# Performance work log

Hardware: AMD Instinct MI355X
Metric: run time of the kernel (lower is better)

## Reference

```python
import jax, jax.numpy as jnp
import numpy as np

N = 30000   # nodes
E = 480000  # edges
IN = 128    # hidden_dim (in_feats)
H = 4       # num_heads
D = 128     # out_feats per head
HD = H * D
NEG_SLOPE = 0.2
BN_EPS = 1e-5


def setup_inputs() -> dict:
    key = jax.random.key(0)
    ks = jax.random.split(key, 12)
    feat = jax.random.normal(ks[0], (N, IN), dtype=jnp.float32)
    src = jax.random.randint(ks[1], (E,), 0, N)
    dst = jax.random.randint(ks[2], (E,), 0, N)
    sc_in = 1.0 / np.sqrt(IN)
    sc_hd = 1.0 / np.sqrt(HD)
    W_fc = jax.random.normal(ks[3], (IN, HD), dtype=jnp.float32) * sc_in
    attn_l = jax.random.normal(ks[4], (H, D), dtype=jnp.float32) * sc_in
    attn_r = jax.random.normal(ks[5], (H, D), dtype=jnp.float32) * sc_in
    W_res = jax.random.normal(ks[6], (IN, HD), dtype=jnp.float32) * sc_in
    bias_gat = jnp.zeros((HD,), dtype=jnp.float32)
    gamma = jnp.ones((HD,), dtype=jnp.float32)
    beta = jnp.zeros((HD,), dtype=jnp.float32)
    W_out = jax.random.normal(ks[7], (HD, IN), dtype=jnp.float32) * sc_hd
    b_out = jnp.zeros((IN,), dtype=jnp.float32)
    return dict(feat=feat, src=src, dst=dst, W_fc=W_fc, attn_l=attn_l,
                attn_r=attn_r, W_res=W_res, bias_gat=bias_gat,
                gamma=gamma, beta=beta, W_out=W_out, b_out=b_out)


def reference(feat, src, dst, W_fc, attn_l, attn_r, W_res, bias_gat,
              gamma, beta, W_out, b_out):
    # --- GATConv (eval mode: dropout off) ---
    h = (feat @ W_fc).reshape(N, H, D)               # projected feats [N,H,D]
    el = jnp.einsum('nhd,hd->nh', h, attn_l)         # [N,H]
    er = jnp.einsum('nhd,hd->nh', h, attn_r)         # [N,H]
    e = el[src] + er[dst]                            # [E,H]
    e = jnp.where(e > 0, e, NEG_SLOPE * e)           # leaky_relu(0.2)
    # segment softmax over edges grouped by destination node
    emax = jax.ops.segment_max(e, dst, num_segments=N)   # [N,H]
    emax = jnp.where(jnp.isfinite(emax), emax, 0.0)      # empty segments
    ex = jnp.exp(e - emax[dst])                          # [E,H]
    denom = jax.ops.segment_sum(ex, dst, num_segments=N) # [N,H]
    a = ex / denom[dst]                                  # [E,H] attention
    msgs = h[src] * a[:, :, None]                        # [E,H,D]
    rst = jax.ops.segment_sum(msgs, dst, num_segments=N) # [N,H,D]
    # residual (in_feats != H*out_feats -> linear res_fc) + bias
    rst = rst + (feat @ W_res).reshape(N, H, D) + bias_gat.reshape(1, H, D)
    # --- fc_out: Flatten -> BatchNorm1d (train stats) -> ReLU -> Linear ---
    x = rst.reshape(N, HD)
    mu = x.mean(axis=0)
    var = x.var(axis=0)
    xn = (x - mu) / jnp.sqrt(var + BN_EPS)
    x = jnp.maximum(gamma * xn + beta, 0.0)
    return x @ W_out + b_out                             # [N, IN]
```

## Files before the change

kernel.cpp:

```cpp
#include <hip/hip_runtime.h>

#define N_  30000
#define E_  480000

typedef short short8 __attribute__((ext_vector_type(8)));
typedef float f32x4  __attribute__((ext_vector_type(4)));
typedef unsigned int u32x4 __attribute__((ext_vector_type(4)));
typedef unsigned int u32x2 __attribute__((ext_vector_type(2)));
union Frag { u32x4 q; short8 v; unsigned short us[8]; };

__device__ __forceinline__ float b2f(unsigned short u){
  union { unsigned int i; float f; } v; v.i = ((unsigned int)u) << 16; return v.f;
}
__device__ __forceinline__ float blo(unsigned int u){
  union { unsigned int i; float f; } v; v.i = u << 16; return v.f;
}
__device__ __forceinline__ float bhi(unsigned int u){
  union { unsigned int i; float f; } v; v.i = u & 0xffff0000u; return v.f;
}
__device__ __forceinline__ unsigned short f2b(float f){
  union { float f; unsigned int u; } v; v.f = f;
  unsigned int u = v.u;
  return (unsigned short)((u + 0x7fffu + ((u >> 16) & 1u)) >> 16);
}

__global__ void k_initconv(const float* __restrict__ Wfc, const float* __restrict__ Wres,
                           const float* __restrict__ Wout, const float* __restrict__ feat,
                           unsigned short* __restrict__ Wt2, unsigned short* __restrict__ WtOut,
                           unsigned short* __restrict__ featb,
                           int* __restrict__ counts, int* __restrict__ cursor){
  int gid = blockIdx.x * 256 + threadIdx.x;
  int stride = gridDim.x * 256;
  if (gid < N_){ counts[gid] = 0; cursor[gid] = 0; }
  const int total1 = 512 * 256;
  const int total2 = 128 * 512;
  for (int i = gid; i < total1 + total2; i += stride){
    if (i < total1){
      int c = i >> 8, k = i & 255;
      float v = (k < 128) ? Wfc[k * 512 + c] : Wres[(k - 128) * 512 + c];
      Wt2[c * 256 + k] = f2b(v);
    } else {
      int j = i - total1;
      int n = j >> 9, k = j & 511;
      WtOut[n * 512 + k] = f2b(Wout[k * 128 + n]);
    }
  }
  for (int i = gid; i < N_ * 128; i += stride)
    featb[i] = f2b(feat[i]);
}

__global__ __launch_bounds__(128) void k_prep(const float* __restrict__ Wfc,
                                              const float* __restrict__ al,
                                              const float* __restrict__ ar,
                                              float* __restrict__ P){
  int idx = blockIdx.x * 128 + threadIdx.x;
  if (idx >= 1024) return;
  int k = idx >> 3, q = idx & 7;
  int h = q & 3;
  const float* a = (q < 4) ? al : ar;
  const float* wr = Wfc + k * 512 + h * 128;
  const float* av = a + h * 128;
  float s = 0.f;
#pragma unroll 4
  for (int d = 0; d < 128; d++) s += wr[d] * av[d];
  P[k * 8 + q] = s;
}

__global__ __launch_bounds__(256) void k_el(const float* __restrict__ feat,
                                            const float* __restrict__ P,
                                            float* __restrict__ el, float* __restrict__ er){
  __shared__ float sF[32 * 132];
  __shared__ float sP[1024];
  int t = threadIdx.x;
  int n0 = blockIdx.x * 32;
  *reinterpret_cast<f32x4*>(&sP[t * 4]) = *reinterpret_cast<const f32x4*>(P + t * 4);
#pragma unroll
  for (int i = 0; i < 4; i++){
    int c = t + i * 256;
    int r = c >> 5, cw = (c & 31) * 4;
    int gn = n0 + r;
    f32x4 v = {0.f, 0.f, 0.f, 0.f};
    if (gn < N_) v = *reinterpret_cast<const f32x4*>(feat + gn * 128 + cw);
    *reinterpret_cast<f32x4*>(&sF[r * 132 + cw]) = v;
  }
  __syncthreads();
  int node = t >> 3, q = t & 7;
  int gn = n0 + node;
  const float* fr = &sF[node * 132];
  float s = 0.f;
#pragma unroll 2
  for (int k = 0; k < 128; k += 4){
    f32x4 fv = *reinterpret_cast<const f32x4*>(fr + k);
#pragma unroll
    for (int j = 0; j < 4; j++) s += fv[j] * sP[(k + j) * 8 + q];
  }
  if (gn < N_){
    if (q < 4) el[gn * 4 + q] = s;
    else       er[gn * 4 + (q - 4)] = s;
  }
}

__global__ void k_hist(const int* __restrict__ dst, int* __restrict__ counts){
  int e = blockIdx.x * 256 + threadIdx.x;
  if (e < E_) atomicAdd(&counts[dst[e]], 1);
}

__global__ __launch_bounds__(1024) void k_scan(const int* __restrict__ counts,
                                               int* __restrict__ offs){
  __shared__ int wsum[16];
  int t = threadIdx.x;
  int lane = t & 63, w = t >> 6;
  int base = t * 32;
  int vals[32];
  int s = 0;
#pragma unroll
  for (int j = 0; j < 32; j++){
    int idx = base + j;
    int v = (idx < N_) ? counts[idx] : 0;
    vals[j] = s;
    s += v;
  }
  int x = s;
  for (int o = 1; o < 64; o <<= 1){
    int y = __shfl_up(x, o);
    if (lane >= o) x += y;
  }
  if (lane == 63) wsum[w] = x;
  __syncthreads();
  if (t < 16){
    int y = wsum[t];
    for (int o = 1; o < 16; o <<= 1){
      int z = __shfl_up(y, o, 16);
      if (t >= o) y += z;
    }
    wsum[t] = y;
  }
  __syncthreads();
  int wbase = (w > 0) ? wsum[w - 1] : 0;
  int ex = wbase + x - s;
#pragma unroll
  for (int j = 0; j < 32; j++){
    int idx = base + j;
    if (idx <= N_) offs[idx] = ex + vals[j];
  }
}

__global__ void k_edge(const int* __restrict__ src, const int* __restrict__ dst,
                       const float* __restrict__ el, const float* __restrict__ er,
                       float* __restrict__ es_s, int* __restrict__ src_s,
                       const int* __restrict__ offs, int* __restrict__ cursor){
  int e = blockIdx.x * 256 + threadIdx.x;
  if (e >= E_) return;
  int s = src[e], d = dst[e];
  f32x4 a = *reinterpret_cast<const f32x4*>(el + s * 4);
  f32x4 b = *reinterpret_cast<const f32x4*>(er + d * 4);
  f32x4 v = a + b;
#pragma unroll
  for (int i = 0; i < 4; i++) v[i] = v[i] > 0.f ? v[i] : 0.2f * v[i];
  int p = atomicAdd(&cursor[d], 1);
  int pos = offs[d] + p;
  *reinterpret_cast<f32x4*>(es_s + pos * 4) = v;
  src_s[pos] = s;
}

__global__ __launch_bounds__(256) void k_soft(const int* __restrict__ offs,
                                              float* __restrict__ es_s){
  int wave = threadIdx.x >> 6, lane = threadIdx.x & 63;
  int n = blockIdx.x * 4 + wave;
  if (n >= N_) return;
  int head = lane >> 4, sub = lane & 15;
  int off0 = offs[n], g = offs[n + 1] - off0;
  float m = -1e30f;
  for (int i = sub; i < g; i += 16)
    m = fmaxf(m, es_s[(off0 + i) * 4 + head]);
  for (int o = 8; o >= 1; o >>= 1) m = fmaxf(m, __shfl_xor(m, o, 16));
  float ss = 0.f;
  for (int i = sub; i < g; i += 16)
    ss += __expf(es_s[(off0 + i) * 4 + head] - m);
  for (int o = 8; o >= 1; o >>= 1) ss += __shfl_xor(ss, o, 16);
  float rd = (ss > 0.f) ? 1.0f / ss : 0.f;
  for (int i = sub; i < g; i += 16){
    int idx = (off0 + i) * 4 + head;
    es_s[idx] = __expf(es_s[idx] - m) * rd;
  }
}

__global__ __launch_bounds__(256) void k_aggrf(const int* __restrict__ offs,
                                               const int* __restrict__ src_s,
                                               const float* __restrict__ w,
                                               const unsigned short* __restrict__ featb,
                                               unsigned short* __restrict__ fagg){
  int wave = threadIdx.x >> 6, lane = threadIdx.x & 63;
  int n = blockIdx.x * 4 + wave;
  if (n >= N_) return;
  int off0 = __builtin_amdgcn_readfirstlane(offs[n]);
  int g = __builtin_amdgcn_readfirstlane(offs[n + 1]) - off0;
  int c0 = lane * 2;
  float acc[4][2] = {};
  int i = 0;
  for (; i + 7 < g; i += 8){
    int s8[8];
    f32x4 w8[8];
    unsigned int p8[8];
#pragma unroll
    for (int u = 0; u < 8; u++) s8[u] = __builtin_amdgcn_readfirstlane(src_s[off0 + i + u]);
#pragma unroll
    for (int u = 0; u < 8; u++) w8[u] = *reinterpret_cast<const f32x4*>(w + (off0 + i + u) * 4);
#pragma unroll
    for (int u = 0; u < 8; u++) p8[u] = *reinterpret_cast<const unsigned int*>(featb + s8[u] * 128 + c0);
#pragma unroll
    for (int u = 0; u < 8; u++){
      float lo = blo(p8[u]), hi = bhi(p8[u]);
#pragma unroll
      for (int h = 0; h < 4; h++){
        acc[h][0] += w8[u][h] * lo;
        acc[h][1] += w8[u][h] * hi;
      }
    }
  }
  for (; i < g; i++){
    int sv = __builtin_amdgcn_readfirstlane(src_s[off0 + i]);
    f32x4 wv = *reinterpret_cast<const f32x4*>(w + (off0 + i) * 4);
    unsigned int pv = *reinterpret_cast<const unsigned int*>(featb + sv * 128 + c0);
    float lo = blo(pv), hi = bhi(pv);
#pragma unroll
    for (int h = 0; h < 4; h++){
      acc[h][0] += wv[h] * lo;
      acc[h][1] += wv[h] * hi;
    }
  }
#pragma unroll
  for (int h = 0; h < 4; h++){
    unsigned int ov = (unsigned int)f2b(acc[h][0]) | ((unsigned int)f2b(acc[h][1]) << 16);
    *reinterpret_cast<unsigned int*>(fagg + n * 512 + h * 128 + c0) = ov;
  }
}

__global__ __launch_bounds__(256) void k_gemmC(const unsigned short* __restrict__ fagg,
                                               const unsigned short* __restrict__ featb,
                                               const unsigned short* __restrict__ Wt2,
                                               const float* __restrict__ bias,
                                               unsigned short* __restrict__ comb){
  __shared__ unsigned short wsl[256 * 40];
  int tid = threadIdx.x;
  int wave = tid >> 6, lane = tid & 63;
  int lrow = lane & 15, quad = lane >> 4;
  int rowbase = blockIdx.x * 64 + wave * 16;
  int colbase = blockIdx.y * 256;
  int h0 = blockIdx.y * 2;
  int arow = rowbase + lrow; if (arow > N_ - 1) arow = N_ - 1;
  const unsigned short* aF = fagg + arow * 512 + h0 * 128;
  const unsigned short* aX = featb + arow * 128;
  f32x4 acc[16] = {};
  for (int kk = 0; kk < 8; kk++){
    __syncthreads();
#pragma unroll
    for (int i = 0; i < 4; i++){
      int c = tid + i * 256;
      int col = c >> 2, w = (c & 3) * 8;
      u32x4 v = *reinterpret_cast<const u32x4*>(Wt2 + (colbase + col) * 256 + kk * 32 + w);
      *reinterpret_cast<u32x4*>(&wsl[col * 40 + w]) = v;
    }
    __syncthreads();
    Frag a0, a1;
    if (kk < 4){
      a0.q = *reinterpret_cast<const u32x4*>(aF + kk * 32 + quad * 8);
      a1.q = *reinterpret_cast<const u32x4*>(aF + 128 + kk * 32 + quad * 8);
    } else {
      a0.q = *reinterpret_cast<const u32x4*>(aX + (kk - 4) * 32 + quad * 8);
      a1.q = a0.q;
    }
#pragma unroll
    for (int s = 0; s < 16; s++){
      Frag b; b.q = *reinterpret_cast<const u32x4*>(&wsl[(s * 16 + lrow) * 40 + quad * 8]);
      acc[s] = __builtin_amdgcn_mfma_f32_16x16x32_bf16(b.v, (s < 8 ? a0.v : a1.v), acc[s], 0, 0, 0);
    }
  }
  int gr = rowbase + lrow;
  if (gr < N_){
    unsigned short* crow = comb + gr * 512 + colbase;
#pragma unroll
    for (int s = 0; s < 16; s++){
      int cb = colbase + s * 16 + quad * 4;
      f32x4 bb = *reinterpret_cast<const f32x4*>(bias + cb);
      u32x2 ov;
#pragma unroll
      for (int d = 0; d < 2; d++){
        float v0 = acc[s][2 * d]     + bb[2 * d];
        float v1 = acc[s][2 * d + 1] + bb[2 * d + 1];
        ov[d] = (unsigned int)f2b(v0) | ((unsigned int)f2b(v1) << 16);
      }
      *reinterpret_cast<u32x2*>(crow + s * 16 + quad * 4) = ov;
    }
  }
}

__global__ __launch_bounds__(256) void k_stats(const unsigned short* __restrict__ comb,
                                               float* __restrict__ psum,
                                               float* __restrict__ psq){
  __shared__ float lsum[4][512];
  __shared__ float lsq[4][512];
  int t = threadIdx.x, lane = t & 63, rg = t >> 6;
  int c0 = lane * 8;
  const int rows = 118;
  int r0 = blockIdx.x * rows;
  int r1 = r0 + rows; if (r1 > N_) r1 = N_;
  float s[8] = {}, q[8] = {};
  for (int r = r0 + rg; r < r1; r += 4){
    u32x4 pv = *reinterpret_cast<const u32x4*>(comb + r * 512 + c0);
#pragma unroll
    for (int d = 0; d < 4; d++){
      float v0 = blo(pv[d]);
      float v1 = bhi(pv[d]);
      s[2*d]   += v0; q[2*d]   += v0 * v0;
      s[2*d+1] += v1; q[2*d+1] += v1 * v1;
    }
  }
#pragma unroll
  for (int d = 0; d < 8; d++){ lsum[rg][c0 + d] = s[d]; lsq[rg][c0 + d] = q[d]; }
  __syncthreads();
#pragma unroll
  for (int half = 0; half < 2; half++){
    int ch = t + half * 256;
    float a = lsum[0][ch] + lsum[1][ch] + lsum[2][ch] + lsum[3][ch];
    float b = lsq[0][ch] + lsq[1][ch] + lsq[2][ch] + lsq[3][ch];
    psum[blockIdx.x * 512 + ch] = a;
    psq[blockIdx.x * 512 + ch] = b;
  }
}

__global__ __launch_bounds__(128) void k_bnfin(const float* __restrict__ psum,
                                               const float* __restrict__ psq,
                                               const float* __restrict__ gamma,
                                               const float* __restrict__ beta,
                                               float* __restrict__ scale,
                                               float* __restrict__ shift){
  int ch = blockIdx.x * 128 + threadIdx.x;
  float s0 = 0.f, s1 = 0.f, s2 = 0.f, s3 = 0.f;
  float q0 = 0.f, q1 = 0.f, q2 = 0.f, q3 = 0.f;
  for (int b = 0; b < 256; b += 4){
    s0 += psum[(b    ) * 512 + ch];
    s1 += psum[(b + 1) * 512 + ch];
    s2 += psum[(b + 2) * 512 + ch];
    s3 += psum[(b + 3) * 512 + ch];
    q0 += psq[(b    ) * 512 + ch];
    q1 += psq[(b + 1) * 512 + ch];
    q2 += psq[(b + 2) * 512 + ch];
    q3 += psq[(b + 3) * 512 + ch];
  }
  float sum = (s0 + s1) + (s2 + s3);
  float sq  = (q0 + q1) + (q2 + q3);
  float mu  = sum / (float)N_;
  float var = sq / (float)N_ - mu * mu;
  float inv = rsqrtf(var + 1e-5f);
  float sc  = gamma[ch] * inv;
  scale[ch] = sc;
  shift[ch] = beta[ch] - mu * sc;
}

__global__ __launch_bounds__(256) void k_gemm2(const unsigned short* __restrict__ comb,
                                               const unsigned short* __restrict__ WtOut,
                                               const float* __restrict__ scale,
                                               const float* __restrict__ shift,
                                               const float* __restrict__ bout,
                                               float* __restrict__ out){
  __shared__ float sc[512], sh[512];
  __shared__ unsigned short wsl[128 * 40];
  int t = threadIdx.x;
  for (int i = t; i < 512; i += 256){ sc[i] = scale[i]; sh[i] = shift[i]; }
  int wave = t >> 6, lane = t & 63, lrow = lane & 15, quad = lane >> 4;
  int rowbase = blockIdx.x * 64 + wave * 16;
  int rr = rowbase + lrow; if (rr > N_ - 1) rr = N_ - 1;
  const unsigned short* arow = comb + rr * 512;
  f32x4 acc[8] = {};
  for (int kk = 0; kk < 16; kk++){
    __syncthreads();
#pragma unroll
    for (int i = 0; i < 2; i++){
      int c = t + i * 256;
      int col = c >> 2, w = (c & 3) * 8;
      u32x4 v = *reinterpret_cast<const u32x4*>(WtOut + col * 512 + kk * 32 + w);
      *reinterpret_cast<u32x4*>(&wsl[col * 40 + w]) = v;
    }
    __syncthreads();
    int base = kk * 32 + quad * 8;
    Frag a; a.q = *reinterpret_cast<const u32x4*>(arow + base);
#pragma unroll
    for (int i2 = 0; i2 < 8; i2++){
      float x = b2f(a.us[i2]);
      x = fmaf(x, sc[base + i2], sh[base + i2]);
      a.us[i2] = f2b(fmaxf(x, 0.0f));
    }
#pragma unroll
    for (int s = 0; s < 8; s++){
      Frag b; b.q = *reinterpret_cast<const u32x4*>(&wsl[(s * 16 + lrow) * 40 + quad * 8]);
      acc[s] = __builtin_amdgcn_mfma_f32_16x16x32_bf16(b.v, a.v, acc[s], 0, 0, 0);
    }
  }
  int gr = rowbase + lrow;
  if (gr < N_){
    float* orow = out + gr * 128;
#pragma unroll
    for (int s = 0; s < 8; s++){
      int cb = s * 16 + quad * 4;
      f32x4 bb = *reinterpret_cast<const f32x4*>(bout + cb);
      f32x4 ov;
#pragma unroll
      for (int j = 0; j < 4; j++) ov[j] = acc[s][j] + bb[j];
      *reinterpret_cast<f32x4*>(orow + cb) = ov;
    }
  }
}

extern "C" void kernel_launch(void* const* d_in, const int* in_sizes, int n_in,
                              void* d_out, int out_size, void* d_ws, size_t ws_size,
                              hipStream_t stream){
  const float* feat  = (const float*)d_in[0];
  const int*   src   = (const int*)d_in[1];
  const int*   dst   = (const int*)d_in[2];
  const float* Wfc   = (const float*)d_in[3];
  const float* al    = (const float*)d_in[4];
  const float* ar    = (const float*)d_in[5];
  const float* Wres  = (const float*)d_in[6];
  const float* bias  = (const float*)d_in[7];
  const float* gamma = (const float*)d_in[8];
  const float* beta  = (const float*)d_in[9];
  const float* Wout  = (const float*)d_in[10];
  const float* bout  = (const float*)d_in[11];
  float* out = (float*)d_out;

  char* ws = (char*)d_ws;
  unsigned short* comb  = (unsigned short*)(ws + 0);
  unsigned short* fagg  = (unsigned short*)(ws + 30720000);
  unsigned short* Wt2   = (unsigned short*)(ws + 61440000);
  unsigned short* WtOut = (unsigned short*)(ws + 61702144);
  float*          el    = (float*)(ws + 61833216);
  float*          er    = (float*)(ws + 62313216);
  float*          es_s  = (float*)(ws + 62793216);
  int*            offs  = (int*)(ws + 70473216);
  int*            counts= (int*)(ws + 70593280);
  int*            cursor= (int*)(ws + 70713280);
  int*            src_s = (int*)(ws + 70833280);
  float*          psum  = (float*)(ws + 72753280);
  float*          psq   = (float*)(ws + 73277568);
  float*          scale = (float*)(ws + 73801856);
  float*          shift = (float*)(ws + 73803904);
  unsigned short* featb = (unsigned short*)(ws + 73805952);
  float*          P     = psum;

  k_initconv<<<640, 256, 0, stream>>>(Wfc, Wres, Wout, feat, Wt2, WtOut, featb,
                                      counts, cursor);
  k_prep<<<8, 128, 0, stream>>>(Wfc, al, ar, P);
  k_hist<<<(E_ + 255) / 256, 256, 0, stream>>>(dst, counts);
  k_scan<<<1, 1024, 0, stream>>>(counts, offs);
  k_el<<<(N_ + 31) / 32, 256, 0, stream>>>(feat, P, el, er);
  k_edge<<<(E_ + 255) / 256, 256, 0, stream>>>(src, dst, el, er, es_s, src_s, offs, cursor);
  k_soft<<<(N_ + 3) / 4, 256, 0, stream>>>(offs, es_s);
  k_aggrf<<<(N_ + 3) / 4, 256, 0, stream>>>(offs, src_s, es_s, featb, fagg);
  dim3 gC((N_ + 63) / 64, 2);
  k_gemmC<<<gC, 256, 0, stream>>>(fagg, featb, Wt2, bias, comb);
  k_stats<<<256, 256, 0, stream>>>(comb, psum, psq);
  k_bnfin<<<4, 128, 0, stream>>>(psum, psq, gamma, beta, scale, shift);
  k_gemm2<<<(N_ + 63) / 64, 256, 0, stream>>>(comb, WtOut, scale, shift, bout, out);
}
```

Baseline: 289.3 us.

## Fuse segment softmax into aggregation and enlarge swizzled weight tiles in GEMMs

Removes the separate softmax kernel by computing per-destination max and sum inside the aggregation kernel. Unnormalized exp weights are cached in shared memory for the first 128 edges and the reciprocal sum is applied once at output. Both GEMM kernels now use 512-thread blocks covering 128 rows and load 128-wide K slabs of weights into XOR-swizzled LDS, with the weight matrices re-laid out to match. This cuts launch count, global passes over edge scores, and barrier frequency, at the cost of more LDS per block and lower occupancy.

```diff
diff --git a/kernel.cpp b/kernel.cpp
--- a/kernel.cpp
+++ b/kernel.cpp
@@ -38,11 +38,11 @@
     if (i < total1){
       int c = i >> 8, k = i & 255;
       float v = (k < 128) ? Wfc[k * 512 + c] : Wres[(k - 128) * 512 + c];
-      Wt2[c * 256 + k] = f2b(v);
+      Wt2[((k >> 7) << 16) + c * 128 + (k & 127)] = f2b(v);
     } else {
       int j = i - total1;
       int n = j >> 9, k = j & 511;
-      WtOut[n * 512 + k] = f2b(Wout[k * 128 + n]);
+      WtOut[((k >> 7) << 14) + n * 128 + (k & 127)] = f2b(Wout[k * 128 + n]);
     }
   }
   for (int i = gid; i < N_ * 128; i += stride)
@@ -163,39 +163,47 @@
   src_s[pos] = s;
 }
 
-__global__ __launch_bounds__(256) void k_soft(const int* __restrict__ offs,
-                                              float* __restrict__ es_s){
-  int wave = threadIdx.x >> 6, lane = threadIdx.x & 63;
-  int n = blockIdx.x * 4 + wave;
-  if (n >= N_) return;
-  int head = lane >> 4, sub = lane & 15;
-  int off0 = offs[n], g = offs[n + 1] - off0;
-  float m = -1e30f;
-  for (int i = sub; i < g; i += 16)
-    m = fmaxf(m, es_s[(off0 + i) * 4 + head]);
-  for (int o = 8; o >= 1; o >>= 1) m = fmaxf(m, __shfl_xor(m, o, 16));
-  float ss = 0.f;
-  for (int i = sub; i < g; i += 16)
-    ss += __expf(es_s[(off0 + i) * 4 + head] - m);
-  for (int o = 8; o >= 1; o >>= 1) ss += __shfl_xor(ss, o, 16);
-  float rd = (ss > 0.f) ? 1.0f / ss : 0.f;
-  for (int i = sub; i < g; i += 16){
-    int idx = (off0 + i) * 4 + head;
-    es_s[idx] = __expf(es_s[idx] - m) * rd;
-  }
-}
-
 __global__ __launch_bounds__(256) void k_aggrf(const int* __restrict__ offs,
                                                const int* __restrict__ src_s,
-                                               const float* __restrict__ w,
+                                               const float* __restrict__ es,
                                                const unsigned short* __restrict__ featb,
                                                unsigned short* __restrict__ fagg){
+  __shared__ float wls[4][512];
   int wave = threadIdx.x >> 6, lane = threadIdx.x & 63;
   int n = blockIdx.x * 4 + wave;
   if (n >= N_) return;
   int off0 = __builtin_amdgcn_readfirstlane(offs[n]);
   int g = __builtin_amdgcn_readfirstlane(offs[n + 1]) - off0;
   int c0 = lane * 2;
+
+  f32x4 m = {-1e30f, -1e30f, -1e30f, -1e30f};
+  for (int i = lane; i < g; i += 64){
+    f32x4 v = *reinterpret_cast<const f32x4*>(es + (off0 + i) * 4);
+#pragma unroll
+    for (int h = 0; h < 4; h++) m[h] = fmaxf(m[h], v[h]);
+  }
+#pragma unroll
+  for (int o = 32; o >= 1; o >>= 1){
+#pragma unroll
+    for (int h = 0; h < 4; h++) m[h] = fmaxf(m[h], __shfl_xor(m[h], o));
+  }
+  f32x4 ssum = {0.f, 0.f, 0.f, 0.f};
+  for (int i = lane; i < g; i += 64){
+    f32x4 v = *reinterpret_cast<const f32x4*>(es + (off0 + i) * 4);
+    f32x4 e;
+#pragma unroll
+    for (int h = 0; h < 4; h++){ e[h] = __expf(v[h] - m[h]); ssum[h] += e[h]; }
+    if (i < 128) *reinterpret_cast<f32x4*>(&wls[wave][i * 4]) = e;
+  }
+#pragma unroll
+  for (int o = 32; o >= 1; o >>= 1){
+#pragma unroll
+    for (int h = 0; h < 4; h++) ssum[h] += __shfl_xor(ssum[h], o);
+  }
+  f32x4 rd;
+#pragma unroll
+  for (int h = 0; h < 4; h++) rd[h] = (ssum[h] > 0.f) ? 1.0f / ssum[h] : 0.f;
+
   float acc[4][2] = {};
   int i = 0;
   for (; i + 7 < g; i += 8){
@@ -205,7 +213,15 @@
 #pragma unroll
     for (int u = 0; u < 8; u++) s8[u] = __builtin_amdgcn_readfirstlane(src_s[off0 + i + u]);
 #pragma unroll
-    for (int u = 0; u < 8; u++) w8[u] = *reinterpret_cast<const f32x4*>(w + (off0 + i + u) * 4);
+    for (int u = 0; u < 8; u++){
+      int ei = i + u;
+      if (ei < 128) w8[u] = *reinterpret_cast<const f32x4*>(&wls[wave][ei * 4]);
+      else {
+        f32x4 v = *reinterpret_cast<const f32x4*>(es + (off0 + ei) * 4);
+#pragma unroll
+        for (int h = 0; h < 4; h++) w8[u][h] = __expf(v[h] - m[h]);
+      }
+    }
 #pragma unroll
     for (int u = 0; u < 8; u++) p8[u] = *reinterpret_cast<const unsigned int*>(featb + s8[u] * 128 + c0);
 #pragma unroll
@@ -220,7 +236,13 @@
   }
   for (; i < g; i++){
     int sv = __builtin_amdgcn_readfirstlane(src_s[off0 + i]);
-    f32x4 wv = *reinterpret_cast<const f32x4*>(w + (off0 + i) * 4);
+    f32x4 wv;
+    if (i < 128) wv = *reinterpret_cast<const f32x4*>(&wls[wave][i * 4]);
+    else {
+      f32x4 v = *reinterpret_cast<const f32x4*>(es + (off0 + i) * 4);
+#pragma unroll
+      for (int h = 0; h < 4; h++) wv[h] = __expf(v[h] - m[h]);
+    }
     unsigned int pv = *reinterpret_cast<const unsigned int*>(featb + sv * 128 + c0);
     float lo = blo(pv), hi = bhi(pv);
 #pragma unroll
@@ -231,49 +253,57 @@
   }
 #pragma unroll
   for (int h = 0; h < 4; h++){
-    unsigned int ov = (unsigned int)f2b(acc[h][0]) | ((unsigned int)f2b(acc[h][1]) << 16);
+    unsigned int ov = (unsigned int)f2b(acc[h][0] * rd[h]) |
+                      ((unsigned int)f2b(acc[h][1] * rd[h]) << 16);
     *reinterpret_cast<unsigned int*>(fagg + n * 512 + h * 128 + c0) = ov;
   }
 }
 
-__global__ __launch_bounds__(256) void k_gemmC(const unsigned short* __restrict__ fagg,
+__global__ __launch_bounds__(512) void k_gemmC(const unsigned short* __restrict__ fagg,
                                                const unsigned short* __restrict__ featb,
                                                const unsigned short* __restrict__ Wt2,
                                                const float* __restrict__ bias,
                                                unsigned short* __restrict__ comb){
-  __shared__ unsigned short wsl[256 * 40];
+  __shared__ unsigned short wsl[256 * 128];
+  char* wb = (char*)wsl;
   int tid = threadIdx.x;
   int wave = tid >> 6, lane = tid & 63;
   int lrow = lane & 15, quad = lane >> 4;
-  int rowbase = blockIdx.x * 64 + wave * 16;
+  int rowbase = blockIdx.x * 128 + wave * 16;
   int colbase = blockIdx.y * 256;
   int h0 = blockIdx.y * 2;
   int arow = rowbase + lrow; if (arow > N_ - 1) arow = N_ - 1;
   const unsigned short* aF = fagg + arow * 512 + h0 * 128;
   const unsigned short* aX = featb + arow * 128;
   f32x4 acc[16] = {};
-  for (int kk = 0; kk < 8; kk++){
+  for (int phase = 0; phase < 2; phase++){
     __syncthreads();
 #pragma unroll
-    for (int i = 0; i < 4; i++){
-      int c = tid + i * 256;
-      int col = c >> 2, w = (c & 3) * 8;
-      u32x4 v = *reinterpret_cast<const u32x4*>(Wt2 + (colbase + col) * 256 + kk * 32 + w);
-      *reinterpret_cast<u32x4*>(&wsl[col * 40 + w]) = v;
+    for (int i = 0; i < 8; i++){
+      int c = tid + i * 512;
+      int col = c >> 4, unit = c & 15;
+      u32x4 v = *reinterpret_cast<const u32x4*>(Wt2 + (phase << 16) + (colbase + col) * 128 + unit * 8);
+      int byte = (col * 256 + unit * 16) ^ ((col & 7) << 4);
+      *reinterpret_cast<u32x4*>(wb + byte) = v;
     }
     __syncthreads();
-    Frag a0, a1;
-    if (kk < 4){
-      a0.q = *reinterpret_cast<const u32x4*>(aF + kk * 32 + quad * 8);
-      a1.q = *reinterpret_cast<const u32x4*>(aF + 128 + kk * 32 + quad * 8);
-    } else {
-      a0.q = *reinterpret_cast<const u32x4*>(aX + (kk - 4) * 32 + quad * 8);
-      a1.q = a0.q;
-    }
-#pragma unroll
-    for (int s = 0; s < 16; s++){
-      Frag b; b.q = *reinterpret_cast<const u32x4*>(&wsl[(s * 16 + lrow) * 40 + quad * 8]);
-      acc[s] = __builtin_amdgcn_mfma_f32_16x16x32_bf16(b.v, (s < 8 ? a0.v : a1.v), acc[s], 0, 0, 0);
+#pragma unroll
+    for (int kk = 0; kk < 4; kk++){
+      Frag a0, a1;
+      if (phase == 0){
+        a0.q = *reinterpret_cast<const u32x4*>(aF + kk * 32 + quad * 8);
+        a1.q = *reinterpret_cast<const u32x4*>(aF + 128 + kk * 32 + quad * 8);
+      } else {
+        a0.q = *reinterpret_cast<const u32x4*>(aX + kk * 32 + quad * 8);
+        a1.q = a0.q;
+      }
+#pragma unroll
+      for (int s = 0; s < 16; s++){
+        int r = s * 16 + lrow;
+        int byte = (r * 256 + kk * 64 + quad * 16) ^ ((r & 7) << 4);
+        Frag b; b.q = *reinterpret_cast<const u32x4*>(wb + byte);
+        acc[s] = __builtin_amdgcn_mfma_f32_16x16x32_bf16(b.v, (s < 8 ? a0.v : a1.v), acc[s], 0, 0, 0);
+      }
     }
   }
   int gr = rowbase + lrow;
@@ -281,8 +311,7 @@
     unsigned short* crow = comb + gr * 512 + colbase;
 #pragma unroll
     for (int s = 0; s < 16; s++){
-      int cb = colbase + s * 16 + quad * 4;
-      f32x4 bb = *reinterpret_cast<const f32x4*>(bias + cb);
+      f32x4 bb = *reinterpret_cast<const f32x4*>(bias + colbase + s * 16 + quad * 4);
       u32x2 ov;
 #pragma unroll
       for (int d = 0; d < 2; d++){
@@ -358,43 +387,50 @@
   shift[ch] = beta[ch] - mu * sc;
 }
 
-__global__ __launch_bounds__(256) void k_gemm2(const unsigned short* __restrict__ comb,
+__global__ __launch_bounds__(512) void k_gemm2(const unsigned short* __restrict__ comb,
                                                const unsigned short* __restrict__ WtOut,
                                                const float* __restrict__ scale,
                                                const float* __restrict__ shift,
                                                const float* __restrict__ bout,
                                                float* __restrict__ out){
   __shared__ float sc[512], sh[512];
-  __shared__ unsigned short wsl[128 * 40];
+  __shared__ unsigned short wsl[128 * 128];
+  char* wb = (char*)wsl;
   int t = threadIdx.x;
-  for (int i = t; i < 512; i += 256){ sc[i] = scale[i]; sh[i] = shift[i]; }
+  sc[t] = scale[t]; sh[t] = shift[t];
   int wave = t >> 6, lane = t & 63, lrow = lane & 15, quad = lane >> 4;
-  int rowbase = blockIdx.x * 64 + wave * 16;
+  int rowbase = blockIdx.x * 128 + wave * 16;
   int rr = rowbase + lrow; if (rr > N_ - 1) rr = N_ - 1;
   const unsigned short* arow = comb + rr * 512;
   f32x4 acc[8] = {};
-  for (int kk = 0; kk < 16; kk++){
+  for (int phase = 0; phase < 4; phase++){
     __syncthreads();
 #pragma unroll
-    for (int i = 0; i < 2; i++){
-      int c = t + i * 256;
-      int col = c >> 2, w = (c & 3) * 8;
-      u32x4 v = *reinterpret_cast<const u32x4*>(WtOut + col * 512 + kk * 32 + w);
-      *reinterpret_cast<u32x4*>(&wsl[col * 40 + w]) = v;
+    for (int i = 0; i < 4; i++){
+      int c = t + i * 512;
+      int col = c >> 4, unit = c & 15;
+      u32x4 v = *reinterpret_cast<const u32x4*>(WtOut + (phase << 14) + col * 128 + unit * 8);
+      int byte = (col * 256 + unit * 16) ^ ((col & 7) << 4);
+      *reinterpret_cast<u32x4*>(wb + byte) = v;
     }
     __syncthreads();
-    int base = kk * 32 + quad * 8;
-    Frag a; a.q = *reinterpret_cast<const u32x4*>(arow + base);
-#pragma unroll
-    for (int i2 = 0; i2 < 8; i2++){
-      float x = b2f(a.us[i2]);
-      x = fmaf(x, sc[base + i2], sh[base + i2]);
-      a.us[i2] = f2b(fmaxf(x, 0.0f));
-    }
-#pragma unroll
-    for (int s = 0; s < 8; s++){
-      Frag b; b.q = *reinterpret_cast<const u32x4*>(&wsl[(s * 16 + lrow) * 40 + quad * 8]);
-      acc[s] = __builtin_amdgcn_mfma_f32_16x16x32_bf16(b.v, a.v, acc[s], 0, 0, 0);
+#pragma unroll
+    for (int kk = 0; kk < 4; kk++){
+      int base = phase * 128 + kk * 32 + quad * 8;
+      Frag a; a.q = *reinterpret_cast<const u32x4*>(arow + base);
+#pragma unroll
+      for (int i2 = 0; i2 < 8; i2++){
+        float x = b2f(a.us[i2]);
+        x = fmaf(x, sc[base + i2], sh[base + i2]);
+        a.us[i2] = f2b(fmaxf(x, 0.0f));
+      }
+#pragma unroll
+      for (int s = 0; s < 8; s++){
+        int r = s * 16 + lrow;
+        int byte = (r * 256 + kk * 64 + quad * 16) ^ ((r & 7) << 4);
+        Frag b; b.q = *reinterpret_cast<const u32x4*>(wb + byte);
+        acc[s] = __builtin_amdgcn_mfma_f32_16x16x32_bf16(b.v, a.v, acc[s], 0, 0, 0);
+      }
     }
   }
   int gr = rowbase + lrow;
@@ -455,11 +491,10 @@
   k_scan<<<1, 1024, 0, stream>>>(counts, offs);
   k_el<<<(N_ + 31) / 32, 256, 0, stream>>>(feat, P, el, er);
   k_edge<<<(E_ + 255) / 256, 256, 0, stream>>>(src, dst, el, er, es_s, src_s, offs, cursor);
-  k_soft<<<(N_ + 3) / 4, 256, 0, stream>>>(offs, es_s);
   k_aggrf<<<(N_ + 3) / 4, 256, 0, stream>>>(offs, src_s, es_s, featb, fagg);
-  dim3 gC((N_ + 63) / 64, 2);
-  k_gemmC<<<gC, 256, 0, stream>>>(fagg, featb, Wt2, bias, comb);
+  dim3 gC((N_ + 127) / 128, 2);
+  k_gemmC<<<gC, 512, 0, stream>>>(fagg, featb, Wt2, bias, comb);
   k_stats<<<256, 256, 0, stream>>>(comb, psum, psq);
   k_bnfin<<<4, 128, 0, stream>>>(psum, psq, gamma, beta, scale, shift);
-  k_gemm2<<<(N_ + 63) / 64, 256, 0, stream>>>(comb, WtOut, scale, shift, bout, out);
-}
+  k_gemm2<<<(N_ + 127) / 128, 512, 0, stream>>>(comb, WtOut, scale, shift, bout, out);
+}
```

New measurement: 286.0 us. Within noise of the previous version (-1.1%).
